# Kernel tuning notes

Hardware: AMD Instinct MI355X
Metric: run time of the kernel (lower is better)

Reference implementation:

```python
import math
import jax, jax.numpy as jnp
import numpy as np

B, S, HID = 2, 2048, 1024
H, D = 16, 64
LOG2E = 1.442695041


def setup_inputs() -> dict:
    key = jax.random.key(0)
    ks = jax.random.split(key, 10)
    init = lambda k, shape, fan_in: jax.random.uniform(k, shape, jnp.float32, -1.0, 1.0) / math.sqrt(fan_in)
    hidden_states = jax.random.normal(ks[0], (B, S, HID), jnp.float32)
    # additive causal mask [B, 1, S, S]: 0 on/below diagonal, large negative above
    neg = jnp.finfo(jnp.float32).min
    causal = jnp.where(jnp.tril(jnp.ones((S, S), bool)), 0.0, neg).astype(jnp.float32)
    attention_mask = jnp.broadcast_to(causal[None, None], (B, 1, S, S))
    return {
        "hidden_states": hidden_states,
        "attention_mask": attention_mask,
        "scaling": jax.random.normal(ks[1], (D,), jnp.float32) * 0.1,
        "q_w": init(ks[2], (H * D, HID), HID),
        "q_b": jnp.zeros((H * D,), jnp.float32),
        "k_w": init(ks[3], (H * D, HID), HID),
        "k_b": jnp.zeros((H * D,), jnp.float32),
        "v_w": init(ks[4], (H * D, HID), HID),
        "v_b": jnp.zeros((H * D,), jnp.float32),
        "o_w": init(ks[5], (HID, H * D), H * D),
        "o_b": jnp.zeros((HID,), jnp.float32),
    }


def reference(hidden_states, attention_mask, scaling, q_w, q_b, k_w, k_b, v_w, v_b, o_w, o_b):
    x = hidden_states  # [B, S, HID]
    def proj(w, b):
        y = jnp.einsum('bsh,oh->bso', x, w) + b          # [B, S, H*D]
        return y.reshape(B, S, H, D).transpose(0, 2, 1, 3)  # [B, H, S, D]
    q = proj(q_w, q_b)
    k = proj(k_w, k_b)
    v = proj(v_w, v_b)
    # learned per-head-dim softplus scale on queries
    scale = jax.nn.softplus(scaling) * (LOG2E / math.sqrt(D))  # [D]
    q = q * scale[None, None, None, :]
    attn = jnp.einsum('bhsd,bhtd->bhst', q, k)  # [B, H, S, S]
    attn = attn + attention_mask
    attn = jax.nn.softmax(attn.astype(jnp.float32), axis=-1).astype(q.dtype)
    # dropout p=0.0 / eval mode: no-op
    out = jnp.einsum('bhst,bhtd->bhsd', attn, v)           # [B, H, S, D]
    out = out.transpose(0, 2, 1, 3).reshape(B, S, H * D)   # [B, S, H*D]
    out = jnp.einsum('bsf,of->bso', out, o_w) + o_b        # [B, S, HID]
    return out, attn
```

## Files before the change

### kernel.cpp

```cpp
#include <hip/hip_runtime.h>
#include <hip/hip_bf16.h>

#define BATCH 2
#define SEQ   2048
#define HIDN  1024
#define NH    16
#define HD    64

typedef __attribute__((ext_vector_type(8))) short short8;
typedef __attribute__((ext_vector_type(4))) float floatx4;
typedef __attribute__((ext_vector_type(8))) unsigned short ushort8;
typedef __attribute__((ext_vector_type(4))) unsigned short ushort4v;

__device__ __forceinline__ unsigned short f2bf(float f) {
    union { float f; unsigned int u; } v; v.f = f;
    unsigned int u = v.u;
    u += 0x7fffu + ((u >> 16) & 1u);
    return (unsigned short)(u >> 16);
}

__device__ __forceinline__ ushort8 pack16(float4 f0, float4 f1) {
    ushort8 r;
    r[0] = f2bf(f0.x); r[1] = f2bf(f0.y); r[2] = f2bf(f0.z); r[3] = f2bf(f0.w);
    r[4] = f2bf(f1.x); r[5] = f2bf(f1.y); r[6] = f2bf(f1.z); r[7] = f2bf(f1.w);
    return r;
}

__global__ __launch_bounds__(256) void qkv_kernel(
    const float* __restrict__ x,
    const float* __restrict__ qw, const float* __restrict__ qbias,
    const float* __restrict__ kw, const float* __restrict__ kbias,
    const float* __restrict__ vw, const float* __restrict__ vbias,
    const float* __restrict__ scaling,
    unsigned short* __restrict__ qo,
    unsigned short* __restrict__ ko,
    unsigned short* __restrict__ vo)
{
    const int z = blockIdx.z;
    const float* w    = (z == 0) ? qw : (z == 1) ? kw : vw;
    const float* bias = (z == 0) ? qbias : (z == 1) ? kbias : vbias;
    unsigned short* dst = (z == 0) ? qo : (z == 1) ? ko : vo;

    const int n0 = blockIdx.x * 128;
    const int m0 = blockIdx.y * 128;
    const int tid  = threadIdx.x;
    const int lane = tid & 63;
    const int wv   = tid >> 6;
    const int nidx = lane & 15;
    const int quad = lane >> 4;

    __shared__ unsigned short As[128][40];
    __shared__ unsigned short Bs[128][40];

    floatx4 acc[2][8];
#pragma unroll
    for (int rt = 0; rt < 2; rt++)
#pragma unroll
        for (int ct = 0; ct < 8; ct++) acc[rt][ct] = (floatx4)0.0f;

    const int srow = tid >> 1;
    const int scol = (tid & 1) * 16;

    for (int k0 = 0; k0 < HIDN; k0 += 32) {
        __syncthreads();
        {
            const float4* g = (const float4*)(x + (size_t)(m0 + srow) * HIDN + k0 + scol);
            float4 f0 = g[0], f1 = g[1], f2 = g[2], f3 = g[3];
            *(ushort8*)&As[srow][scol]     = pack16(f0, f1);
            *(ushort8*)&As[srow][scol + 8] = pack16(f2, f3);
        }
        {
            const float4* g = (const float4*)(w + (size_t)(n0 + srow) * HIDN + k0 + scol);
            float4 f0 = g[0], f1 = g[1], f2 = g[2], f3 = g[3];
            *(ushort8*)&Bs[srow][scol]     = pack16(f0, f1);
            *(ushort8*)&Bs[srow][scol + 8] = pack16(f2, f3);
        }
        __syncthreads();

        short8 a[2], bb[8];
#pragma unroll
        for (int rt = 0; rt < 2; rt++)
            a[rt] = *(const short8*)&As[wv * 32 + rt * 16 + nidx][quad * 8];
#pragma unroll
        for (int ct = 0; ct < 8; ct++)
            bb[ct] = *(const short8*)&Bs[ct * 16 + nidx][quad * 8];
#pragma unroll
        for (int rt = 0; rt < 2; rt++)
#pragma unroll
            for (int ct = 0; ct < 8; ct++)
                acc[rt][ct] = __builtin_amdgcn_mfma_f32_16x16x32_bf16(a[rt], bb[ct], acc[rt][ct], 0, 0, 0);
    }

    const float sconst = 1.442695041f / 8.0f;
#pragma unroll
    for (int ct = 0; ct < 8; ct++) {
        int col = n0 + ct * 16 + nidx;
        float bcol = bias[col];
        float mult = 1.0f;
        if (z == 0) {
            float sc = scaling[col & (HD - 1)];
            mult = __logf(1.0f + __expf(sc)) * sconst;
        }
#pragma unroll
        for (int rt = 0; rt < 2; rt++) {
#pragma unroll
            for (int rg = 0; rg < 4; rg++) {
                int row = m0 + wv * 32 + rt * 16 + quad * 4 + rg;
                float val = (acc[rt][ct][rg] + bcol) * mult;
                int b_ = row >> 11, s_ = row & (SEQ - 1);
                int h_ = col >> 6,  d_ = col & (HD - 1);
                dst[((size_t)(b_ * NH + h_) * SEQ + s_) * HD + d_] = f2bf(val);
            }
        }
    }
}

__global__ __launch_bounds__(256) void attn_kernel(
    const unsigned short* __restrict__ q,
    const unsigned short* __restrict__ k,
    const unsigned short* __restrict__ v,
    float* __restrict__ attn,
    unsigned short* __restrict__ ctx)
{
    const int h  = blockIdx.y;
    const int b  = blockIdx.z;
    const int tid  = threadIdx.x;
    const int lane = tid & 63;
    const int wv   = tid >> 6;
    const int nidx = lane & 15;
    const int quad = lane >> 4;

    const unsigned short* qg = q + (size_t)((b * NH + h) * SEQ) * HD;
    const unsigned short* kg = k + (size_t)((b * NH + h) * SEQ) * HD;
    const unsigned short* vg = v + (size_t)((b * NH + h) * SEQ) * HD;
    float* ag = attn + (size_t)(b * NH + h) * SEQ * SEQ;

    __shared__ unsigned short Vs[2][64][72];
    __shared__ unsigned short Ps[64][72];

    const int srow = tid >> 2;
    const int sseg = tid & 3;
    const int qrowl = wv * 16 + nidx;
    const int crow0 = wv * 16 + quad * 4;

    for (int rep = 0; rep < 2; rep++) {
        const int qt = rep ? (31 - (int)blockIdx.x) : (int)blockIdx.x;
        __syncthreads();

        const unsigned short* qrow = qg + (size_t)(qt * 64 + qrowl) * HD;
        const short8 qb0 = *(const short8*)(qrow + quad * 8);
        const short8 qb1 = *(const short8*)(qrow + 32 + quad * 8);
        const int qrowg = qt * 64 + qrowl;

        float psum = 0.0f;
        for (int kt = 0; kt <= qt; kt++) {
            const unsigned short* kbase = kg + (size_t)(kt * 64) * HD;
            const bool diag = (kt == qt);
#pragma unroll
            for (int ct = 0; ct < 4; ct++) {
                const unsigned short* krow = kbase + (ct * 16 + nidx) * HD;
                short8 ak0 = *(const short8*)(krow + quad * 8);
                short8 ak1 = *(const short8*)(krow + 32 + quad * 8);
                floatx4 sacc = (floatx4)0.0f;
                __builtin_amdgcn_s_setprio(1);
                sacc = __builtin_amdgcn_mfma_f32_16x16x32_bf16(ak0, qb0, sacc, 0, 0, 0);
                sacc = __builtin_amdgcn_mfma_f32_16x16x32_bf16(ak1, qb1, sacc, 0, 0, 0);
                __builtin_amdgcn_s_setprio(0);
                const int kcol0 = kt * 64 + ct * 16 + quad * 4;
#pragma unroll
                for (int rg = 0; rg < 4; rg++) {
                    float e = __expf(sacc[rg]);
                    if (diag && kcol0 + rg > qrowg) e = 0.0f;
                    psum += e;
                }
            }
        }

        psum += __shfl_xor(psum, 16);
        psum += __shfl_xor(psum, 32);
        const float invl = 1.0f / psum;

        floatx4 oacc[4];
#pragma unroll
        for (int ct = 0; ct < 4; ct++) oacc[ct] = (floatx4)0.0f;

        {
            const uint4* g = (const uint4*)(vg + (size_t)(srow) * HD);
            uint4 u0 = g[sseg], u1 = g[sseg + 4];
            union { uint4 u; unsigned short s[8]; } w0, w1;
            w0.u = u0; w1.u = u1;
#pragma unroll
            for (int j = 0; j < 8; j++) Vs[0][sseg * 8 + j][srow]      = w0.s[j];
#pragma unroll
            for (int j = 0; j < 8; j++) Vs[0][sseg * 8 + 32 + j][srow] = w1.s[j];
        }

        for (int kt = 0; kt <= qt; kt++) {
            __syncthreads();
            if (kt < qt) {
                const uint4* g = (const uint4*)(vg + (size_t)((kt + 1) * 64 + srow) * HD);
                uint4 u0 = g[sseg], u1 = g[sseg + 4];
                union { uint4 u; unsigned short s[8]; } w0, w1;
                w0.u = u0; w1.u = u1;
                const int nb = (kt + 1) & 1;
#pragma unroll
                for (int j = 0; j < 8; j++) Vs[nb][sseg * 8 + j][srow]      = w0.s[j];
#pragma unroll
                for (int j = 0; j < 8; j++) Vs[nb][sseg * 8 + 32 + j][srow] = w1.s[j];
            }

            const unsigned short* kbase = kg + (size_t)(kt * 64) * HD;
            const bool diag = (kt == qt);
            const int cb = kt & 1;
#pragma unroll
            for (int ct = 0; ct < 4; ct++) {
                const unsigned short* krow = kbase + (ct * 16 + nidx) * HD;
                short8 ak0 = *(const short8*)(krow + quad * 8);
                short8 ak1 = *(const short8*)(krow + 32 + quad * 8);
                floatx4 sacc = (floatx4)0.0f;
                __builtin_amdgcn_s_setprio(1);
                sacc = __builtin_amdgcn_mfma_f32_16x16x32_bf16(ak0, qb0, sacc, 0, 0, 0);
                sacc = __builtin_amdgcn_mfma_f32_16x16x32_bf16(ak1, qb1, sacc, 0, 0, 0);
                __builtin_amdgcn_s_setprio(0);
                const int kcol0 = kt * 64 + ct * 16 + quad * 4;
                floatx4 av;
                ushort4v pb;
#pragma unroll
                for (int rg = 0; rg < 4; rg++) {
                    float e = __expf(sacc[rg]);
                    if (diag && kcol0 + rg > qrowg) e = 0.0f;
                    av[rg] = e * invl;
                    pb[rg] = f2bf(e);
                }
                __builtin_nontemporal_store(av, (floatx4*)&ag[(size_t)qrowg * SEQ + kcol0]);
                *(ushort4v*)&Ps[qrowl][ct * 16 + quad * 4] = pb;
            }

            __builtin_amdgcn_s_setprio(1);
#pragma unroll
            for (int ki = 0; ki < 2; ki++) {
                short8 pa = *(const short8*)&Ps[qrowl][ki * 32 + quad * 8];
#pragma unroll
                for (int ct = 0; ct < 4; ct++) {
                    short8 vb = *(const short8*)&Vs[cb][ct * 16 + nidx][ki * 32 + quad * 8];
                    oacc[ct] = __builtin_amdgcn_mfma_f32_16x16x32_bf16(pa, vb, oacc[ct], 0, 0, 0);
                }
            }
            __builtin_amdgcn_s_setprio(0);
        }

        const int zc0 = (qt + 1) * 64;
        if (zc0 < SEQ) {
            const floatx4 zz = (floatx4)0.0f;
            const int zw4 = (SEQ - zc0) >> 2;
            const int total = 64 * zw4;
            for (int i = tid; i < total; i += 256) {
                int r = i / zw4;
                int c = zc0 + (i - r * zw4) * 4;
                __builtin_nontemporal_store(zz, (floatx4*)&ag[(size_t)(qt * 64 + r) * SEQ + c]);
            }
        }

#pragma unroll
        for (int ct = 0; ct < 4; ct++) {
#pragma unroll
            for (int rg = 0; rg < 4; rg++) {
                int rowg = qt * 64 + crow0 + rg;
                int d = ct * 16 + nidx;
                float iv = __shfl(invl, quad * 4 + rg);
                float val = oacc[ct][rg] * iv;
                ctx[((size_t)(b * SEQ + rowg) * NH + h) * HD + d] = f2bf(val);
            }
        }
    }
}

__global__ __launch_bounds__(256) void oproj_kernel(
    const unsigned short* __restrict__ ctx,
    const float* __restrict__ ow, const float* __restrict__ ob,
    float* __restrict__ out)
{
    const int n0 = blockIdx.x * 128;
    const int m0 = blockIdx.y * 128;
    const int tid  = threadIdx.x;
    const int lane = tid & 63;
    const int wv   = tid >> 6;
    const int nidx = lane & 15;
    const int quad = lane >> 4;

    __shared__ unsigned short As[128][40];
    __shared__ unsigned short Bs[128][40];

    floatx4 acc[2][8];
#pragma unroll
    for (int rt = 0; rt < 2; rt++)
#pragma unroll
        for (int ct = 0; ct < 8; ct++) acc[rt][ct] = (floatx4)0.0f;

    const int srow = tid >> 1;
    const int scol = (tid & 1) * 16;

    for (int k0 = 0; k0 < HIDN; k0 += 32) {
        __syncthreads();
        {
            const uint4* g = (const uint4*)(ctx + (size_t)(m0 + srow) * HIDN + k0 + scol);
            uint4 u0 = g[0], u1 = g[1];
            *(uint4*)&As[srow][scol]     = u0;
            *(uint4*)&As[srow][scol + 8] = u1;
        }
        {
            const float4* g = (const float4*)(ow + (size_t)(n0 + srow) * HIDN + k0 + scol);
            float4 f0 = g[0], f1 = g[1], f2 = g[2], f3 = g[3];
            *(ushort8*)&Bs[srow][scol]     = pack16(f0, f1);
            *(ushort8*)&Bs[srow][scol + 8] = pack16(f2, f3);
        }
        __syncthreads();

        short8 a[2], bb[8];
#pragma unroll
        for (int rt = 0; rt < 2; rt++)
            a[rt] = *(const short8*)&As[wv * 32 + rt * 16 + nidx][quad * 8];
#pragma unroll
        for (int ct = 0; ct < 8; ct++)
            bb[ct] = *(const short8*)&Bs[ct * 16 + nidx][quad * 8];
#pragma unroll
        for (int rt = 0; rt < 2; rt++)
#pragma unroll
            for (int ct = 0; ct < 8; ct++)
                acc[rt][ct] = __builtin_amdgcn_mfma_f32_16x16x32_bf16(a[rt], bb[ct], acc[rt][ct], 0, 0, 0);
    }

#pragma unroll
    for (int ct = 0; ct < 8; ct++) {
        int col = n0 + ct * 16 + nidx;
        float bcol = ob[col];
#pragma unroll
        for (int rt = 0; rt < 2; rt++) {
#pragma unroll
            for (int rg = 0; rg < 4; rg++) {
                int row = m0 + wv * 32 + rt * 16 + quad * 4 + rg;
                out[(size_t)row * HIDN + col] = acc[rt][ct][rg] + bcol;
            }
        }
    }
}

extern "C" void kernel_launch(void* const* d_in, const int* in_sizes, int n_in,
                              void* d_out, int out_size, void* d_ws, size_t ws_size,
                              hipStream_t stream) {
    const float* x       = (const float*)d_in[0];
    const float* scaling = (const float*)d_in[2];
    const float* qw = (const float*)d_in[3];
    const float* qb = (const float*)d_in[4];
    const float* kw = (const float*)d_in[5];
    const float* kb = (const float*)d_in[6];
    const float* vw = (const float*)d_in[7];
    const float* vb = (const float*)d_in[8];
    const float* ow = (const float*)d_in[9];
    const float* ob = (const float*)d_in[10];

    float* out  = (float*)d_out;
    float* attn = out + (size_t)BATCH * SEQ * HIDN;

    const size_t per = (size_t)BATCH * NH * SEQ * HD;
    unsigned short* qbuf = (unsigned short*)d_ws;
    unsigned short* kbuf = qbuf + per;
    unsigned short* vbuf = kbuf + per;
    unsigned short* ctxb = vbuf + per;

    qkv_kernel<<<dim3(8, 32, 3), 256, 0, stream>>>(
        x, qw, qb, kw, kb, vw, vb, scaling, qbuf, kbuf, vbuf);
    attn_kernel<<<dim3(16, NH, BATCH), 256, 0, stream>>>(
        qbuf, kbuf, vbuf, attn, ctxb);
    oproj_kernel<<<dim3(8, 32), 256, 0, stream>>>(
        ctxb, ow, ob, out);
}
```

Before: 812.8 us.

## Drop softmax row-sum pass; write unnormalized probs and rescale in a separate kernel

The attention kernel no longer runs a separate QK^T plus exp pass just to get the softmax denominators. It accumulates row sums during the main pass, writes unnormalized probabilities, and stores the inverse sums to a workspace buffer. A new rescale kernel then rereads the causal lower triangle of the attention matrix and multiplies each row by its inverse sum. The log2(e) factor is folded into the query scale so exp2f can replace __expf. The trade is that half the QK and exp work goes away, but the lower triangle of attn now takes an extra global read and write.

```diff
diff --git a/kernel.cpp b/kernel.cpp
--- a/kernel.cpp
+++ b/kernel.cpp
@@ -91,7 +91,6 @@
                 acc[rt][ct] = __builtin_amdgcn_mfma_f32_16x16x32_bf16(a[rt], bb[ct], acc[rt][ct], 0, 0, 0);
     }
 
-    const float sconst = 1.442695041f / 8.0f;
 #pragma unroll
     for (int ct = 0; ct < 8; ct++) {
         int col = n0 + ct * 16 + nidx;
@@ -99,7 +98,7 @@
         float mult = 1.0f;
         if (z == 0) {
             float sc = scaling[col & (HD - 1)];
-            mult = __logf(1.0f + __expf(sc)) * sconst;
+            mult = __logf(1.0f + __expf(sc)) * 0.26017112f;
         }
 #pragma unroll
         for (int rt = 0; rt < 2; rt++) {
@@ -120,7 +119,8 @@
     const unsigned short* __restrict__ k,
     const unsigned short* __restrict__ v,
     float* __restrict__ attn,
-    unsigned short* __restrict__ ctx)
+    unsigned short* __restrict__ ctx,
+    float* __restrict__ invl_g)
 {
     const int h  = blockIdx.y;
     const int b  = blockIdx.z;
@@ -134,6 +134,7 @@
     const unsigned short* kg = k + (size_t)((b * NH + h) * SEQ) * HD;
     const unsigned short* vg = v + (size_t)((b * NH + h) * SEQ) * HD;
     float* ag = attn + (size_t)(b * NH + h) * SEQ * SEQ;
+    float* ig = invl_g + (size_t)(b * NH + h) * SEQ;
 
     __shared__ unsigned short Vs[2][64][72];
     __shared__ unsigned short Ps[64][72];
@@ -153,33 +154,6 @@
         const int qrowg = qt * 64 + qrowl;
 
         float psum = 0.0f;
-        for (int kt = 0; kt <= qt; kt++) {
-            const unsigned short* kbase = kg + (size_t)(kt * 64) * HD;
-            const bool diag = (kt == qt);
-#pragma unroll
-            for (int ct = 0; ct < 4; ct++) {
-                const unsigned short* krow = kbase + (ct * 16 + nidx) * HD;
-                short8 ak0 = *(const short8*)(krow + quad * 8);
-                short8 ak1 = *(const short8*)(krow + 32 + quad * 8);
-                floatx4 sacc = (floatx4)0.0f;
-                __builtin_amdgcn_s_setprio(1);
-                sacc = __builtin_amdgcn_mfma_f32_16x16x32_bf16(ak0, qb0, sacc, 0, 0, 0);
-                sacc = __builtin_amdgcn_mfma_f32_16x16x32_bf16(ak1, qb1, sacc, 0, 0, 0);
-                __builtin_amdgcn_s_setprio(0);
-                const int kcol0 = kt * 64 + ct * 16 + quad * 4;
-#pragma unroll
-                for (int rg = 0; rg < 4; rg++) {
-                    float e = __expf(sacc[rg]);
-                    if (diag && kcol0 + rg > qrowg) e = 0.0f;
-                    psum += e;
-                }
-            }
-        }
-
-        psum += __shfl_xor(psum, 16);
-        psum += __shfl_xor(psum, 32);
-        const float invl = 1.0f / psum;
-
         floatx4 oacc[4];
 #pragma unroll
         for (int ct = 0; ct < 4; ct++) oacc[ct] = (floatx4)0.0f;
@@ -227,10 +201,11 @@
                 ushort4v pb;
 #pragma unroll
                 for (int rg = 0; rg < 4; rg++) {
-                    float e = __expf(sacc[rg]);
+                    float e = exp2f(sacc[rg]);
                     if (diag && kcol0 + rg > qrowg) e = 0.0f;
-                    av[rg] = e * invl;
+                    av[rg] = e;
                     pb[rg] = f2bf(e);
+                    psum += e;
                 }
                 __builtin_nontemporal_store(av, (floatx4*)&ag[(size_t)qrowg * SEQ + kcol0]);
                 *(ushort4v*)&Ps[qrowl][ct * 16 + quad * 4] = pb;
@@ -248,6 +223,11 @@
             }
             __builtin_amdgcn_s_setprio(0);
         }
+
+        psum += __shfl_xor(psum, 16);
+        psum += __shfl_xor(psum, 32);
+        const float invl = 1.0f / psum;
+        if (quad == 0) ig[qrowg] = invl;
 
         const int zc0 = (qt + 1) * 64;
         if (zc0 < SEQ) {
@@ -270,6 +250,39 @@
                 float iv = __shfl(invl, quad * 4 + rg);
                 float val = oacc[ct][rg] * iv;
                 ctx[((size_t)(b * SEQ + rowg) * NH + h) * HD + d] = f2bf(val);
+            }
+        }
+    }
+}
+
+__global__ __launch_bounds__(256) void rescale_kernel(
+    float* __restrict__ attn, const float* __restrict__ invl_g)
+{
+    const int h = blockIdx.y;
+    const int b = blockIdx.z;
+    const int tid  = threadIdx.x;
+    const int lane = tid & 63;
+    const int wv   = tid >> 6;
+    float* ag = attn + (size_t)(b * NH + h) * SEQ * SEQ;
+    const float* ig = invl_g + (size_t)(b * NH + h) * SEQ;
+
+    __shared__ float iv[64];
+
+    for (int rep = 0; rep < 2; rep++) {
+        const int qt = rep ? (31 - (int)blockIdx.x) : (int)blockIdx.x;
+        __syncthreads();
+        if (tid < 64) iv[tid] = ig[qt * 64 + tid];
+        __syncthreads();
+        const int w4 = 16 * (qt + 1);
+#pragma unroll 1
+        for (int rr = 0; rr < 16; rr++) {
+            const int r = wv * 16 + rr;
+            const float s = iv[r];
+            floatx4* rowp = (floatx4*)(ag + (size_t)(qt * 64 + r) * SEQ);
+            for (int c4 = lane; c4 < w4; c4 += 64) {
+                floatx4 vv = __builtin_nontemporal_load(rowp + c4);
+                vv *= s;
+                __builtin_nontemporal_store(vv, rowp + c4);
             }
         }
     }
@@ -367,11 +380,14 @@
     unsigned short* kbuf = qbuf + per;
     unsigned short* vbuf = kbuf + per;
     unsigned short* ctxb = vbuf + per;
+    float* invlb = (float*)(ctxb + per);
 
     qkv_kernel<<<dim3(8, 32, 3), 256, 0, stream>>>(
         x, qw, qb, kw, kb, vw, vb, scaling, qbuf, kbuf, vbuf);
     attn_kernel<<<dim3(16, NH, BATCH), 256, 0, stream>>>(
-        qbuf, kbuf, vbuf, attn, ctxb);
+        qbuf, kbuf, vbuf, attn, ctxb, invlb);
+    rescale_kernel<<<dim3(16, NH, BATCH), 256, 0, stream>>>(
+        attn, invlb);
     oproj_kernel<<<dim3(8, 32), 256, 0, stream>>>(
         ctxb, ow, ob, out);
 }
```

Result: slower. 953.8 us (+17.3%).

## Pre-convert inputs and weights to bf16 once, retile projection GEMMs smaller

Applied to the files above, without the earlier changes.

Adds a conversion kernel that turns x and all projection weights into bf16 once, so the QKV and output GEMMs load bf16 directly instead of reconverting fp32 tiles in every block. The GEMM tiles shrink (64-wide N, and 64x64 for the output projection) to launch more blocks. The softmax exponent switches to exp2f, with the q scale absorbing the extra log2e factor. This adds a kernel launch and extra workspace traffic.

```diff
diff --git a/kernel.cpp b/kernel.cpp
--- a/kernel.cpp
+++ b/kernel.cpp
@@ -26,22 +26,42 @@
     return r;
 }
 
+__global__ __launch_bounds__(256) void convert_kernel(
+    const float* __restrict__ x,
+    const float* __restrict__ qw, const float* __restrict__ kw,
+    const float* __restrict__ vw, const float* __restrict__ ow,
+    unsigned short* __restrict__ xb,
+    unsigned short* __restrict__ wb,
+    unsigned short* __restrict__ owb)
+{
+    const int bid = blockIdx.x;
+    const float* src; unsigned short* dst; size_t base;
+    if (bid < 2048)      { src = x;  dst = xb;            base = (size_t)bid * 2048; }
+    else if (bid < 2560) { src = qw; dst = wb;            base = (size_t)(bid - 2048) * 2048; }
+    else if (bid < 3072) { src = kw; dst = wb + 1048576;  base = (size_t)(bid - 2560) * 2048; }
+    else if (bid < 3584) { src = vw; dst = wb + 2097152;  base = (size_t)(bid - 3072) * 2048; }
+    else                 { src = ow; dst = owb;           base = (size_t)(bid - 3584) * 2048; }
+    const size_t i = base + (size_t)threadIdx.x * 8;
+    const float4* g = (const float4*)(src + i);
+    *(ushort8*)(dst + i) = pack16(g[0], g[1]);
+}
+
 __global__ __launch_bounds__(256) void qkv_kernel(
-    const float* __restrict__ x,
-    const float* __restrict__ qw, const float* __restrict__ qbias,
-    const float* __restrict__ kw, const float* __restrict__ kbias,
-    const float* __restrict__ vw, const float* __restrict__ vbias,
+    const unsigned short* __restrict__ xb,
+    const unsigned short* __restrict__ wb,
+    const float* __restrict__ qbias, const float* __restrict__ kbias,
+    const float* __restrict__ vbias,
     const float* __restrict__ scaling,
     unsigned short* __restrict__ qo,
     unsigned short* __restrict__ ko,
     unsigned short* __restrict__ vo)
 {
     const int z = blockIdx.z;
-    const float* w    = (z == 0) ? qw : (z == 1) ? kw : vw;
+    const unsigned short* w = wb + (size_t)z * HIDN * HIDN;
     const float* bias = (z == 0) ? qbias : (z == 1) ? kbias : vbias;
     unsigned short* dst = (z == 0) ? qo : (z == 1) ? ko : vo;
 
-    const int n0 = blockIdx.x * 128;
+    const int n0 = blockIdx.x * 64;
     const int m0 = blockIdx.y * 128;
     const int tid  = threadIdx.x;
     const int lane = tid & 63;
@@ -50,56 +70,52 @@
     const int quad = lane >> 4;
 
     __shared__ unsigned short As[128][40];
-    __shared__ unsigned short Bs[128][40];
-
-    floatx4 acc[2][8];
+    __shared__ unsigned short Bs[64][40];
+
+    floatx4 acc[2][4];
 #pragma unroll
     for (int rt = 0; rt < 2; rt++)
 #pragma unroll
-        for (int ct = 0; ct < 8; ct++) acc[rt][ct] = (floatx4)0.0f;
-
-    const int srow = tid >> 1;
-    const int scol = (tid & 1) * 16;
+        for (int ct = 0; ct < 4; ct++) acc[rt][ct] = (floatx4)0.0f;
+
+    const int srowA = tid >> 1, scolA = (tid & 1) * 16;
+    const int srowB = tid >> 2, scolB = (tid & 3) * 8;
 
     for (int k0 = 0; k0 < HIDN; k0 += 32) {
         __syncthreads();
         {
-            const float4* g = (const float4*)(x + (size_t)(m0 + srow) * HIDN + k0 + scol);
-            float4 f0 = g[0], f1 = g[1], f2 = g[2], f3 = g[3];
-            *(ushort8*)&As[srow][scol]     = pack16(f0, f1);
-            *(ushort8*)&As[srow][scol + 8] = pack16(f2, f3);
-        }
-        {
-            const float4* g = (const float4*)(w + (size_t)(n0 + srow) * HIDN + k0 + scol);
-            float4 f0 = g[0], f1 = g[1], f2 = g[2], f3 = g[3];
-            *(ushort8*)&Bs[srow][scol]     = pack16(f0, f1);
-            *(ushort8*)&Bs[srow][scol + 8] = pack16(f2, f3);
-        }
-        __syncthreads();
-
-        short8 a[2], bb[8];
+            const uint4* g = (const uint4*)(xb + (size_t)(m0 + srowA) * HIDN + k0 + scolA);
+            *(uint4*)&As[srowA][scolA]     = g[0];
+            *(uint4*)&As[srowA][scolA + 8] = g[1];
+        }
+        {
+            const uint4* g = (const uint4*)(w + (size_t)(n0 + srowB) * HIDN + k0 + scolB);
+            *(uint4*)&Bs[srowB][scolB] = g[0];
+        }
+        __syncthreads();
+
+        short8 a[2], bb[4];
 #pragma unroll
         for (int rt = 0; rt < 2; rt++)
             a[rt] = *(const short8*)&As[wv * 32 + rt * 16 + nidx][quad * 8];
 #pragma unroll
-        for (int ct = 0; ct < 8; ct++)
+        for (int ct = 0; ct < 4; ct++)
             bb[ct] = *(const short8*)&Bs[ct * 16 + nidx][quad * 8];
 #pragma unroll
         for (int rt = 0; rt < 2; rt++)
 #pragma unroll
-            for (int ct = 0; ct < 8; ct++)
+            for (int ct = 0; ct < 4; ct++)
                 acc[rt][ct] = __builtin_amdgcn_mfma_f32_16x16x32_bf16(a[rt], bb[ct], acc[rt][ct], 0, 0, 0);
     }
 
-    const float sconst = 1.442695041f / 8.0f;
-#pragma unroll
-    for (int ct = 0; ct < 8; ct++) {
+#pragma unroll
+    for (int ct = 0; ct < 4; ct++) {
         int col = n0 + ct * 16 + nidx;
         float bcol = bias[col];
         float mult = 1.0f;
         if (z == 0) {
             float sc = scaling[col & (HD - 1)];
-            mult = __logf(1.0f + __expf(sc)) * sconst;
+            mult = __logf(1.0f + __expf(sc)) * 0.26017112f;
         }
 #pragma unroll
         for (int rt = 0; rt < 2; rt++) {
@@ -169,7 +185,7 @@
                 const int kcol0 = kt * 64 + ct * 16 + quad * 4;
 #pragma unroll
                 for (int rg = 0; rg < 4; rg++) {
-                    float e = __expf(sacc[rg]);
+                    float e = exp2f(sacc[rg]);
                     if (diag && kcol0 + rg > qrowg) e = 0.0f;
                     psum += e;
                 }
@@ -227,7 +243,7 @@
                 ushort4v pb;
 #pragma unroll
                 for (int rg = 0; rg < 4; rg++) {
-                    float e = __expf(sacc[rg]);
+                    float e = exp2f(sacc[rg]);
                     if (diag && kcol0 + rg > qrowg) e = 0.0f;
                     av[rg] = e * invl;
                     pb[rg] = f2bf(e);
@@ -277,70 +293,56 @@
 
 __global__ __launch_bounds__(256) void oproj_kernel(
     const unsigned short* __restrict__ ctx,
-    const float* __restrict__ ow, const float* __restrict__ ob,
+    const unsigned short* __restrict__ owb, const float* __restrict__ ob,
     float* __restrict__ out)
 {
-    const int n0 = blockIdx.x * 128;
-    const int m0 = blockIdx.y * 128;
+    const int n0 = blockIdx.x * 64;
+    const int m0 = blockIdx.y * 64;
     const int tid  = threadIdx.x;
     const int lane = tid & 63;
     const int wv   = tid >> 6;
     const int nidx = lane & 15;
     const int quad = lane >> 4;
 
-    __shared__ unsigned short As[128][40];
-    __shared__ unsigned short Bs[128][40];
-
-    floatx4 acc[2][8];
-#pragma unroll
-    for (int rt = 0; rt < 2; rt++)
-#pragma unroll
-        for (int ct = 0; ct < 8; ct++) acc[rt][ct] = (floatx4)0.0f;
-
-    const int srow = tid >> 1;
-    const int scol = (tid & 1) * 16;
+    __shared__ unsigned short As[64][40];
+    __shared__ unsigned short Bs[64][40];
+
+    floatx4 acc[4];
+#pragma unroll
+    for (int ct = 0; ct < 4; ct++) acc[ct] = (floatx4)0.0f;
+
+    const int srow = tid >> 2, scol = (tid & 3) * 8;
 
     for (int k0 = 0; k0 < HIDN; k0 += 32) {
         __syncthreads();
         {
             const uint4* g = (const uint4*)(ctx + (size_t)(m0 + srow) * HIDN + k0 + scol);
-            uint4 u0 = g[0], u1 = g[1];
-            *(uint4*)&As[srow][scol]     = u0;
-            *(uint4*)&As[srow][scol + 8] = u1;
-        }
-        {
-            const float4* g = (const float4*)(ow + (size_t)(n0 + srow) * HIDN + k0 + scol);
-            float4 f0 = g[0], f1 = g[1], f2 = g[2], f3 = g[3];
-            *(ushort8*)&Bs[srow][scol]     = pack16(f0, f1);
-            *(ushort8*)&Bs[srow][scol + 8] = pack16(f2, f3);
-        }
-        __syncthreads();
-
-        short8 a[2], bb[8];
-#pragma unroll
-        for (int rt = 0; rt < 2; rt++)
-            a[rt] = *(const short8*)&As[wv * 32 + rt * 16 + nidx][quad * 8];
-#pragma unroll
-        for (int ct = 0; ct < 8; ct++)
+            *(uint4*)&As[srow][scol] = g[0];
+        }
+        {
+            const uint4* g = (const uint4*)(owb + (size_t)(n0 + srow) * HIDN + k0 + scol);
+            *(uint4*)&Bs[srow][scol] = g[0];
+        }
+        __syncthreads();
+
+        short8 a = *(const short8*)&As[wv * 16 + nidx][quad * 8];
+        short8 bb[4];
+#pragma unroll
+        for (int ct = 0; ct < 4; ct++)
             bb[ct] = *(const short8*)&Bs[ct * 16 + nidx][quad * 8];
 #pragma unroll
-        for (int rt = 0; rt < 2; rt++)
-#pragma unroll
-            for (int ct = 0; ct < 8; ct++)
-                acc[rt][ct] = __builtin_amdgcn_mfma_f32_16x16x32_bf16(a[rt], bb[ct], acc[rt][ct], 0, 0, 0);
-    }
-
-#pragma unroll
-    for (int ct = 0; ct < 8; ct++) {
+        for (int ct = 0; ct < 4; ct++)
+            acc[ct] = __builtin_amdgcn_mfma_f32_16x16x32_bf16(a, bb[ct], acc[ct], 0, 0, 0);
+    }
+
+#pragma unroll
+    for (int ct = 0; ct < 4; ct++) {
         int col = n0 + ct * 16 + nidx;
         float bcol = ob[col];
 #pragma unroll
-        for (int rt = 0; rt < 2; rt++) {
-#pragma unroll
-            for (int rg = 0; rg < 4; rg++) {
-                int row = m0 + wv * 32 + rt * 16 + quad * 4 + rg;
-                out[(size_t)row * HIDN + col] = acc[rt][ct][rg] + bcol;
-            }
+        for (int rg = 0; rg < 4; rg++) {
+            int row = m0 + wv * 16 + quad * 4 + rg;
+            out[(size_t)row * HIDN + col] = acc[ct][rg] + bcol;
         }
     }
 }
@@ -367,11 +369,16 @@
     unsigned short* kbuf = qbuf + per;
     unsigned short* vbuf = kbuf + per;
     unsigned short* ctxb = vbuf + per;
-
-    qkv_kernel<<<dim3(8, 32, 3), 256, 0, stream>>>(
-        x, qw, qb, kw, kb, vw, vb, scaling, qbuf, kbuf, vbuf);
+    unsigned short* xb   = ctxb + per;
+    unsigned short* wbb  = xb + per;
+    unsigned short* owb  = wbb + (size_t)3 * HIDN * HIDN;
+
+    convert_kernel<<<dim3(4096), 256, 0, stream>>>(
+        x, qw, kw, vw, ow, xb, wbb, owb);
+    qkv_kernel<<<dim3(16, 32, 3), 256, 0, stream>>>(
+        xb, wbb, qb, kb, vb, scaling, qbuf, kbuf, vbuf);
     attn_kernel<<<dim3(16, NH, BATCH), 256, 0, stream>>>(
         qbuf, kbuf, vbuf, attn, ctxb);
-    oproj_kernel<<<dim3(8, 32), 256, 0, stream>>>(
-        ctxb, ow, ob, out);
-}
+    oproj_kernel<<<dim3(16, 64), 256, 0, stream>>>(
+        ctxb, owb, ob, out);
+}
```

Result: faster. 786.3 us (-3.3%).
